# Performance work log

Hardware: AMD Instinct MI355X
Metric: run time of the kernel (lower is better)

Reference implementation:

```python
import jax, jax.numpy as jnp
import numpy as np
from jax.ops import segment_sum, segment_max

B, L, D, H, DK, NL, V, FF = 8, 256, 256, 8, 32, 4, 2048, 1024
N = B * L
EPS = 1e-5


def _ln(x, g, b):
    m = jnp.mean(x, -1, keepdims=True)
    v = jnp.var(x, -1, keepdims=True)
    return (x - m) * jax.lax.rsqrt(v + EPS) * g + b


def setup_inputs() -> dict:
    key = jax.random.key(0)
    ks = list(jax.random.split(key, 16))
    # causal decoder-decoder edges, sorted by destination (DGL 'dd' eids)
    dst_seq = np.repeat(np.arange(L), np.arange(L) + 1)
    src_seq = np.concatenate([np.arange(j + 1) for j in range(L)])
    src = jnp.asarray(np.concatenate([src_seq + b * L for b in range(B)]), jnp.int32)
    dst = jnp.asarray(np.concatenate([dst_seq + b * L for b in range(B)]), jnp.int32)
    tokens = jax.random.randint(ks[0], (N,), 0, V)
    positions = jnp.tile(jnp.arange(L), B)  # tgt[1]
    s = 0.02
    nrm = lambda k, sh: jax.random.normal(k, sh, jnp.float32) * s
    return {
        'tokens': tokens, 'positions': positions, 'src': src, 'dst': dst,
        'value_tab': nrm(ks[1], (V, D)),
        'coord_tab': nrm(ks[2], (3, D)),
        'pos_tab': nrm(ks[3], (L, D)),
        'ln1_g': jnp.ones((NL, D), jnp.float32), 'ln1_b': jnp.zeros((NL, D), jnp.float32),
        'Wq': nrm(ks[4], (NL, D, D)), 'Wk': nrm(ks[5], (NL, D, D)),
        'Wv': nrm(ks[6], (NL, D, D)), 'Wo': nrm(ks[7], (NL, D, D)),
        'ln2_g': jnp.ones((NL, D), jnp.float32), 'ln2_b': jnp.zeros((NL, D), jnp.float32),
        'W1': nrm(ks[8], (NL, D, FF)), 'b1': jnp.zeros((NL, FF), jnp.float32),
        'W2': nrm(ks[9], (NL, FF, D)), 'b2': jnp.zeros((NL, D), jnp.float32),
        'lnf_g': jnp.ones((D,), jnp.float32), 'lnf_b': jnp.zeros((D,), jnp.float32),
        'Wgen': nrm(ks[10], (D, V)), 'bgen': jnp.zeros((V,), jnp.float32),
    }


def reference(tokens, positions, src, dst, value_tab, coord_tab, pos_tab,
              ln1_g, ln1_b, Wq, Wk, Wv, Wo, ln2_g, ln2_b,
              W1, b1, W2, b2, lnf_g, lnf_b, Wgen, bgen):
    # embeddings: value*sqrt(d) + coord(pos%3) + pos(pos//3)
    x = value_tab[tokens] * jnp.sqrt(jnp.float32(D)) \
        + coord_tab[positions % 3] + pos_tab[positions // 3]
    inv_sqrt_dk = 1.0 / jnp.sqrt(jnp.float32(DK))
    for i in range(NL):
        # pre_func: layernorm + qkv projection, split heads
        xn = _ln(x, ln1_g[i], ln1_b[i])
        q = (xn @ Wq[i]).reshape(N, H, DK)
        k = (xn @ Wk[i]).reshape(N, H, DK)
        v = (xn @ Wv[i]).reshape(N, H, DK)
        # apply_edges(u_dot_v): per-edge, per-head score
        score = jnp.einsum('ehd,ehd->eh', k[src], q[dst]) * inv_sqrt_dk  # [E,H]
        # edge_softmax over edges grouped by destination node
        m = jax.lax.stop_gradient(
            segment_max(score, dst, num_segments=N, indices_are_sorted=True))
        a = jnp.exp(score - m[dst])
        denom = segment_sum(a, dst, num_segments=N, indices_are_sorted=True)
        alpha = a / denom[dst]  # [E,H]
        # send_and_recv(u_mul_e -> sum): softmax-weighted aggregation
        z = segment_sum(v[src] * alpha[..., None], dst,
                        num_segments=N, indices_are_sorted=True).reshape(N, D)
        # post_func: output proj + residual, then FFN sublayer
        x = x + z @ Wo[i]
        xn2 = _ln(x, ln2_g[i], ln2_b[i])
        x = x + (jax.nn.relu(xn2 @ W1[i] + b1[i]) @ W2[i] + b2[i])
    x = _ln(x, lnf_g, lnf_b)
    return jax.nn.log_softmax(x @ Wgen + bgen, axis=-1)  # generator
```

## Files before the change

### kernel.cpp

```cpp
#include <hip/hip_runtime.h>
#include <hip/hip_bf16.h>
#include <math.h>

constexpr int B_ = 8, L_ = 256, D_ = 256, H_ = 8, DK_ = 32, NL_ = 4, V_ = 2048, FF_ = 1024;
constexpr int N_ = B_ * L_;
constexpr float EPS_ = 1e-5f;
constexpr int LDW_ = 56;

typedef short bf16x8 __attribute__((ext_vector_type(8)));
typedef float f32x4 __attribute__((ext_vector_type(4)));
typedef _Float16 f16x4 __attribute__((ext_vector_type(4)));

__device__ __forceinline__ short f2b(float f) {
    union { __hip_bfloat16 h; short s; } u;
    u.h = __float2bfloat16(f);
    return u.s;
}

__global__ void transpose_all(const float* __restrict__ Wq, const float* __restrict__ Wk,
                              const float* __restrict__ Wv, const float* __restrict__ Wo,
                              const float* __restrict__ W1, const float* __restrict__ W2,
                              const float* __restrict__ Wgen,
                              short* __restrict__ wqT, short* __restrict__ wkT,
                              short* __restrict__ wvT, short* __restrict__ woT,
                              short* __restrict__ w1T, short* __restrict__ w2T,
                              short* __restrict__ wgT,
                              const int* __restrict__ tokens, const int* __restrict__ positions,
                              const float* __restrict__ vtab, const float* __restrict__ ctab,
                              const float* __restrict__ ptab, float* __restrict__ x) {
    __shared__ float tile[32][33];
    int id = blockIdx.x;
    if (id >= 3584) {
        int n = id - 3584;
        int d = threadIdx.y * 32 + threadIdx.x;
        int tok = tokens[n], p = positions[n];
        x[n * D_ + d] = vtab[tok * D_ + d] * 16.0f + ctab[(p % 3) * D_ + d] + ptab[(p / 3) * D_ + d];
        return;
    }
    const float* src;
    short* dst;
    int K, Nn, tx, ty;
    if (id < 1024) {
        int m = id >> 8, rem = id & 255, layer = rem >> 6, tt = rem & 63;
        K = 256; Nn = 256; tx = tt & 7; ty = tt >> 3;
        size_t off = (size_t)layer * 256 * 256;
        if (m == 0) { src = Wq + off; dst = wqT + off; }
        else if (m == 1) { src = Wk + off; dst = wkT + off; }
        else if (m == 2) { src = Wv + off; dst = wvT + off; }
        else { src = Wo + off; dst = woT + off; }
    } else if (id < 2048) {
        int rem = id - 1024, layer = rem >> 8, tt = rem & 255;
        K = 256; Nn = 1024; tx = tt & 31; ty = tt >> 5;
        size_t off = (size_t)layer * 256 * 1024;
        src = W1 + off; dst = w1T + off;
    } else if (id < 3072) {
        int rem = id - 2048, layer = rem >> 8, tt = rem & 255;
        K = 1024; Nn = 256; tx = tt & 7; ty = tt >> 3;
        size_t off = (size_t)layer * 1024 * 256;
        src = W2 + off; dst = w2T + off;
    } else {
        int tt = id - 3072;
        K = 256; Nn = 2048; tx = tt & 63; ty = tt >> 6;
        src = Wgen; dst = wgT;
    }
    int n0 = tx * 32, k0 = ty * 32;
    int x_ = threadIdx.x, y_ = threadIdx.y;
#pragma unroll
    for (int i = 0; i < 32; i += 8)
        tile[y_ + i][x_] = src[(size_t)(k0 + y_ + i) * Nn + n0 + x_];
    __syncthreads();
#pragma unroll
    for (int i = 0; i < 32; i += 8)
        dst[(size_t)(n0 + y_ + i) * K + k0 + x_] = f2b(tile[x_][y_ + i]);
}

__device__ __forceinline__ int4 pack8(const float* v) {
    union { short s[8]; int4 q; } u;
#pragma unroll
    for (int j = 0; j < 8; ++j) u.s[j] = f2b(v[j]);
    return u.q;
}

template <int EPI, bool HAS_BIAS>
__device__ __forceinline__ void gemm_epilogue(f32x4 acc00, f32x4 acc01, f32x4 acc10, f32x4 acc11,
                                              const float* __restrict__ bias, float* __restrict__ Cf,
                                              short* __restrict__ Cb, int Nout, int kz,
                                              int m0, int n0, int mo, int no, int quad, int r) {
#pragma unroll
    for (int i = 0; i < 2; ++i) {
#pragma unroll
        for (int j = 0; j < 2; ++j) {
            f32x4 acc = (i == 0) ? (j == 0 ? acc00 : acc01) : (j == 0 ? acc10 : acc11);
            int col = n0 + no + j * 16 + r;
            float bval = HAS_BIAS ? bias[col] : 0.f;
#pragma unroll
            for (int p = 0; p < 4; ++p) {
                int row = m0 + mo + i * 16 + quad * 4 + p;
                float v = acc[p];
                if (EPI == 1) {
                    Cb[(size_t)row * Nout + col] = f2b(fmaxf(v + bval, 0.f));
                } else if (EPI == 2) {
                    float add = v + ((HAS_BIAS && kz == 0) ? bval : 0.f);
                    atomicAdd(&Cf[(size_t)row * Nout + col], add);
                } else if (EPI == 3) {
                    Cf[(size_t)row * Nout + col] = v + bval;
                } else if (EPI == 4) {
                    Cb[(size_t)row * Nout + col] = f2b(v);
                } else {
                    ((_Float16*)Cb)[(size_t)row * Nout + col] = (_Float16)v;
                }
            }
        }
    }
}

template <int EPI, bool HAS_BIAS>
__device__ __forceinline__ void gemm_body(const short* __restrict__ A, const short* __restrict__ Bt,
                                          const float* __restrict__ bias, float* __restrict__ Cf,
                                          short* __restrict__ Cb, int M, int K, int Nout,
                                          int kbeg, int kend, int kz) {
    __shared__ short As[2][64][LDW_];
    __shared__ short Bs[2][64][LDW_];
    int t = threadIdx.x;
    int m0 = blockIdx.x * 64, n0 = blockIdx.y * 64;
    int sr = t >> 2, sc = (t & 3) * 8;
    int lane = t & 63, w = t >> 6;
    int mo = (w & 1) * 32, no = (w >> 1) * 32;
    int quad = lane >> 4, r = lane & 15;
    f32x4 acc00 = {}, acc01 = {}, acc10 = {}, acc11 = {};
    const short* Ap = &A[(size_t)(m0 + sr) * K + sc];
    const short* Bp = &Bt[(size_t)(n0 + sr) * K + sc];
    int4 av = *(const int4*)(Ap + kbeg);
    int4 bv = *(const int4*)(Bp + kbeg);
    *(int4*)&As[0][sr][sc] = av;
    *(int4*)&Bs[0][sr][sc] = bv;
    if (kbeg + 32 < kend) {
        av = *(const int4*)(Ap + kbeg + 32);
        bv = *(const int4*)(Bp + kbeg + 32);
    }
    __syncthreads();
    int p = 0;
    for (int k0 = kbeg; k0 < kend; k0 += 32, p ^= 1) {
        if (k0 + 32 < kend) {
            *(int4*)&As[p ^ 1][sr][sc] = av;
            *(int4*)&Bs[p ^ 1][sr][sc] = bv;
            if (k0 + 64 < kend) {
                av = *(const int4*)(Ap + k0 + 64);
                bv = *(const int4*)(Bp + k0 + 64);
            }
        }
        bf16x8 a0 = *(const bf16x8*)&As[p][mo + r][quad * 8];
        bf16x8 a1 = *(const bf16x8*)&As[p][mo + 16 + r][quad * 8];
        bf16x8 b0 = *(const bf16x8*)&Bs[p][no + r][quad * 8];
        bf16x8 b1 = *(const bf16x8*)&Bs[p][no + 16 + r][quad * 8];
        acc00 = __builtin_amdgcn_mfma_f32_16x16x32_bf16(a0, b0, acc00, 0, 0, 0);
        acc01 = __builtin_amdgcn_mfma_f32_16x16x32_bf16(a0, b1, acc01, 0, 0, 0);
        acc10 = __builtin_amdgcn_mfma_f32_16x16x32_bf16(a1, b0, acc10, 0, 0, 0);
        acc11 = __builtin_amdgcn_mfma_f32_16x16x32_bf16(a1, b1, acc11, 0, 0, 0);
        if (k0 + 32 < kend) __syncthreads();
    }
    gemm_epilogue<EPI, HAS_BIAS>(acc00, acc01, acc10, acc11, bias, Cf, Cb, Nout, kz,
                                 m0, n0, mo, no, quad, r);
}

template <int EPI, bool HAS_BIAS>
__device__ __forceinline__ void gemm_ln_body(const float* __restrict__ X,
                                             const float* __restrict__ lg, const float* __restrict__ lb,
                                             const short* __restrict__ Bt,
                                             const float* __restrict__ bias, float* __restrict__ Cf,
                                             short* __restrict__ Cb, int Nout) {
    __shared__ short As[2][64][LDW_];
    __shared__ short Bs[2][64][LDW_];
    __shared__ float gs[256], bs_[256];
    int t = threadIdx.x;
    int m0 = blockIdx.x * 64, n0 = blockIdx.y * 64;
    int sr = t >> 2, sc = (t & 3) * 8;
    int lane = t & 63, w = t >> 6;
    int mo = (w & 1) * 32, no = (w >> 1) * 32;
    int quad = lane >> 4, r = lane & 15;

    float xv[64];
    const float* xp = &X[(size_t)(m0 + sr) * 256 + sc];
#pragma unroll
    for (int c = 0; c < 8; ++c) {
        *(float4*)&xv[c * 8] = *(const float4*)(xp + c * 32);
        *(float4*)&xv[c * 8 + 4] = *(const float4*)(xp + c * 32 + 4);
    }
    const short* Bp = &Bt[(size_t)(n0 + sr) * 256 + sc];
    int4 bv = *(const int4*)Bp;
    gs[t] = lg[t];
    bs_[t] = lb[t];

    float s1 = 0.f, s2 = 0.f;
#pragma unroll
    for (int j = 0; j < 64; ++j) {
        s1 += xv[j];
        s2 += xv[j] * xv[j];
    }
    s1 += __shfl_xor(s1, 1, 64); s1 += __shfl_xor(s1, 2, 64);
    s2 += __shfl_xor(s2, 1, 64); s2 += __shfl_xor(s2, 2, 64);
    float mean = s1 * (1.0f / 256.0f);
    float inv = rsqrtf(s2 * (1.0f / 256.0f) - mean * mean + EPS_);
    __syncthreads();

    int4 a_regs[8];
#pragma unroll
    for (int c = 0; c < 8; ++c) {
        float tmp[8];
#pragma unroll
        for (int j = 0; j < 8; ++j)
            tmp[j] = (xv[c * 8 + j] - mean) * inv * gs[c * 32 + sc + j] + bs_[c * 32 + sc + j];
        a_regs[c] = pack8(tmp);
    }

    *(int4*)&As[0][sr][sc] = a_regs[0];
    *(int4*)&Bs[0][sr][sc] = bv;
    bv = *(const int4*)(Bp + 32);
    __syncthreads();

    f32x4 acc00 = {}, acc01 = {}, acc10 = {}, acc11 = {};
#pragma unroll
    for (int c = 0; c < 8; ++c) {
        int p = c & 1;
        if (c + 1 < 8) {
            *(int4*)&As[p ^ 1][sr][sc] = a_regs[c + 1];
            *(int4*)&Bs[p ^ 1][sr][sc] = bv;
            if (c + 2 < 8) bv = *(const int4*)(Bp + (c + 2) * 32);
        }
        bf16x8 a0 = *(const bf16x8*)&As[p][mo + r][quad * 8];
        bf16x8 a1 = *(const bf16x8*)&As[p][mo + 16 + r][quad * 8];
        bf16x8 b0 = *(const bf16x8*)&Bs[p][no + r][quad * 8];
        bf16x8 b1 = *(const bf16x8*)&Bs[p][no + 16 + r][quad * 8];
        acc00 = __builtin_amdgcn_mfma_f32_16x16x32_bf16(a0, b0, acc00, 0, 0, 0);
        acc01 = __builtin_amdgcn_mfma_f32_16x16x32_bf16(a0, b1, acc01, 0, 0, 0);
        acc10 = __builtin_amdgcn_mfma_f32_16x16x32_bf16(a1, b0, acc10, 0, 0, 0);
        acc11 = __builtin_amdgcn_mfma_f32_16x16x32_bf16(a1, b1, acc11, 0, 0, 0);
        if (c + 1 < 8) __syncthreads();
    }
    gemm_epilogue<EPI, HAS_BIAS>(acc00, acc01, acc10, acc11, bias, Cf, Cb, Nout, 0,
                                 m0, n0, mo, no, quad, r);
}

__global__ __launch_bounds__(256) void gemm_ln_qkv(const float* __restrict__ X,
                                                   const float* __restrict__ lg, const float* __restrict__ lb,
                                                   const short* __restrict__ wq, const short* __restrict__ wk,
                                                   const short* __restrict__ wv,
                                                   short* __restrict__ q, short* __restrict__ k,
                                                   short* __restrict__ v) {
    if (blockIdx.z == 0)
        gemm_ln_body<4, false>(X, lg, lb, wq, nullptr, nullptr, q, D_);
    else if (blockIdx.z == 1)
        gemm_ln_body<4, false>(X, lg, lb, wk, nullptr, nullptr, k, D_);
    else
        gemm_ln_body<5, false>(X, lg, lb, wv, nullptr, nullptr, v, D_);
}

__global__ __launch_bounds__(256) void gemm_ln_relu(const float* __restrict__ X,
                                                    const float* __restrict__ lg, const float* __restrict__ lb,
                                                    const short* __restrict__ Bt, const float* __restrict__ bias,
                                                    short* __restrict__ C) {
    gemm_ln_body<1, true>(X, lg, lb, Bt, bias, nullptr, C, FF_);
}

__global__ __launch_bounds__(256) void gemm_ln_bias(const float* __restrict__ X,
                                                    const float* __restrict__ lg, const float* __restrict__ lb,
                                                    const short* __restrict__ Bt, const float* __restrict__ bias,
                                                    float* __restrict__ C) {
    gemm_ln_body<3, true>(X, lg, lb, Bt, bias, C, nullptr, V_);
}

template <int SPLITK, bool HAS_BIAS>
__global__ __launch_bounds__(256) void gemm_accum(const short* __restrict__ A, const short* __restrict__ Bt,
                                                  const float* __restrict__ bias, float* __restrict__ C,
                                                  int M, int K, int Nout) {
    int Kp = K / SPLITK;
    int kz = blockIdx.z;
    gemm_body<2, HAS_BIAS>(A, Bt, bias, C, nullptr, M, K, Nout, kz * Kp, kz * Kp + Kp, kz);
}

__global__ __launch_bounds__(64) void attn_kernel(const short* __restrict__ q,
                                                  const short* __restrict__ k,
                                                  const _Float16* __restrict__ v,
                                                  short* __restrict__ z) {
    int blk = blockIdx.x;
    int bh = blk & 63;
    int qt = 15 - (blk >> 6);
    int b = bh >> 3, h = bh & 7;
    int lane = threadIdx.x;
    int r = lane & 15, quad = lane >> 4;
    int row0 = b * L_;

    bf16x8 qf = *(const bf16x8*)&q[(size_t)(row0 + qt * 16 + r) * D_ + h * DK_ + quad * 8];
    f32x4 O0 = {}, O1 = {};
    float mA = -1e30f, den = 0.f;
    int nk = qt + 1;

    bf16x8 kf = *(const bf16x8*)&k[(size_t)(row0 + r) * D_ + h * DK_ + quad * 8];
    f16x4 va, vb;
    {
        const _Float16* vp = v + (size_t)(row0 + quad * 4) * D_ + h * DK_;
#pragma unroll
        for (int i = 0; i < 4; ++i) {
            va[i] = vp[(size_t)i * D_ + r];
            vb[i] = vp[(size_t)i * D_ + 16 + r];
        }
    }
    for (int kt = 0; kt < nk; ++kt) {
        bf16x8 kf_n = kf;
        f16x4 va_n = va, vb_n = vb;
        if (kt + 1 < nk) {
            kf_n = *(const bf16x8*)&k[(size_t)(row0 + (kt + 1) * 16 + r) * D_ + h * DK_ + quad * 8];
            const _Float16* vp = v + (size_t)(row0 + (kt + 1) * 16 + quad * 4) * D_ + h * DK_;
#pragma unroll
            for (int i = 0; i < 4; ++i) {
                va_n[i] = vp[(size_t)i * D_ + r];
                vb_n[i] = vp[(size_t)i * D_ + 16 + r];
            }
        }
        f32x4 zero = {};
        f32x4 s = __builtin_amdgcn_mfma_f32_16x16x32_bf16(kf, qf, zero, 0, 0, 0);
#pragma unroll
        for (int i2 = 0; i2 < 4; ++i2) s[i2] *= 0.17677669529663687f;
        if (kt == qt) {
#pragma unroll
            for (int i2 = 0; i2 < 4; ++i2)
                if (quad * 4 + i2 > r) s[i2] = -1e30f;
        }
        float tmax = fmaxf(fmaxf(s[0], s[1]), fmaxf(s[2], s[3]));
        tmax = fmaxf(tmax, __shfl_xor(tmax, 16, 64));
        tmax = fmaxf(tmax, __shfl_xor(tmax, 32, 64));
        float mn = fmaxf(mA, tmax);
        float alpha = __expf(mA - mn);
        mA = mn;
        float p0 = __expf(s[0] - mn), p1 = __expf(s[1] - mn);
        float p2 = __expf(s[2] - mn), p3 = __expf(s[3] - mn);
        float ts = (p0 + p1) + (p2 + p3);
        ts += __shfl_xor(ts, 16, 64);
        ts += __shfl_xor(ts, 32, 64);
        den = den * alpha + ts;
        f16x4 pf;
        pf[0] = (_Float16)p0; pf[1] = (_Float16)p1; pf[2] = (_Float16)p2; pf[3] = (_Float16)p3;
        float al[4];
#pragma unroll
        for (int i2 = 0; i2 < 4; ++i2) al[i2] = __shfl(alpha, quad * 4 + i2, 64);
#pragma unroll
        for (int i2 = 0; i2 < 4; ++i2) { O0[i2] *= al[i2]; O1[i2] *= al[i2]; }
        O0 = __builtin_amdgcn_mfma_f32_16x16x16f16(pf, va, O0, 0, 0, 0);
        O1 = __builtin_amdgcn_mfma_f32_16x16x16f16(pf, vb, O1, 0, 0, 0);
        kf = kf_n; va = va_n; vb = vb_n;
    }
#pragma unroll
    for (int i2 = 0; i2 < 4; ++i2) {
        float inv = 1.0f / __shfl(den, quad * 4 + i2, 64);
        int rowz = row0 + qt * 16 + quad * 4 + i2;
        z[(size_t)rowz * D_ + h * DK_ + r] = f2b(O0[i2] * inv);
        z[(size_t)rowz * D_ + h * DK_ + 16 + r] = f2b(O1[i2] * inv);
    }
}

__global__ void lsm_kernel(float* __restrict__ logits) {
    __shared__ float rm[4], rs[4];
    int row = blockIdx.x, t = threadIdx.x;
    float* p = logits + (size_t)row * V_;
    float vals[8];
    float mx = -INFINITY;
#pragma unroll
    for (int i = 0; i < 8; ++i) {
        vals[i] = p[t + i * 256];
        mx = fmaxf(mx, vals[i]);
    }
#pragma unroll
    for (int off = 32; off; off >>= 1) mx = fmaxf(mx, __shfl_xor(mx, off, 64));
    int w = t >> 6;
    if ((t & 63) == 0) rm[w] = mx;
    __syncthreads();
    mx = fmaxf(fmaxf(rm[0], rm[1]), fmaxf(rm[2], rm[3]));
    float s = 0.f;
#pragma unroll
    for (int i = 0; i < 8; ++i) s += __expf(vals[i] - mx);
#pragma unroll
    for (int off = 32; off; off >>= 1) s += __shfl_xor(s, off, 64);
    if ((t & 63) == 0) rs[w] = s;
    __syncthreads();
    s = rs[0] + rs[1] + rs[2] + rs[3];
    float lse = mx + logf(s);
#pragma unroll
    for (int i = 0; i < 8; ++i) p[t + i * 256] = vals[i] - lse;
}

extern "C" void kernel_launch(void* const* d_in, const int* in_sizes, int n_in,
                              void* d_out, int out_size, void* d_ws, size_t ws_size,
                              hipStream_t stream) {
    const int* tokens = (const int*)d_in[0];
    const int* positions = (const int*)d_in[1];
    const float* vtab = (const float*)d_in[4];
    const float* ctab = (const float*)d_in[5];
    const float* ptab = (const float*)d_in[6];
    const float* ln1_g = (const float*)d_in[7];
    const float* ln1_b = (const float*)d_in[8];
    const float* Wq = (const float*)d_in[9];
    const float* Wk = (const float*)d_in[10];
    const float* Wv = (const float*)d_in[11];
    const float* Wo = (const float*)d_in[12];
    const float* ln2_g = (const float*)d_in[13];
    const float* ln2_b = (const float*)d_in[14];
    const float* W1 = (const float*)d_in[15];
    const float* b1 = (const float*)d_in[16];
    const float* W2 = (const float*)d_in[17];
    const float* b2 = (const float*)d_in[18];
    const float* lnf_g = (const float*)d_in[19];
    const float* lnf_b = (const float*)d_in[20];
    const float* Wgen = (const float*)d_in[21];
    const float* bgen = (const float*)d_in[22];

    char* p = (char*)d_ws;
    float* x = (float*)p;      p += (size_t)N_ * D_ * 4;
    short* qb = (short*)p;     p += (size_t)N_ * D_ * 4;
    short* kb = (short*)p;     p += (size_t)N_ * D_ * 4;
    short* vbh = (short*)p;    p += (size_t)N_ * D_ * 4;
    short* zbb = (short*)p;    p += (size_t)N_ * D_ * 2;
    short* hbb = (short*)p;    p += (size_t)N_ * FF_ * 2;
    short* wqT = (short*)p;    p += (size_t)NL_ * D_ * D_ * 2;
    short* wkT = (short*)p;    p += (size_t)NL_ * D_ * D_ * 2;
    short* wvT = (short*)p;    p += (size_t)NL_ * D_ * D_ * 2;
    short* woT = (short*)p;    p += (size_t)NL_ * D_ * D_ * 2;
    short* w1T = (short*)p;    p += (size_t)NL_ * D_ * FF_ * 2;
    short* w2T = (short*)p;    p += (size_t)NL_ * FF_ * D_ * 2;
    short* wgT = (short*)p;    p += (size_t)D_ * V_ * 2;
    float* out = (float*)d_out;

    dim3 tb(32, 8);
    transpose_all<<<5632, tb, 0, stream>>>(Wq, Wk, Wv, Wo, W1, W2, Wgen,
                                           wqT, wkT, wvT, woT, w1T, w2T, wgT,
                                           tokens, positions, vtab, ctab, ptab, x);

    dim3 gQKV(N_ / 64, D_ / 64, 3);
    dim3 gWo(N_ / 64, D_ / 64, 2);
    dim3 gW1(N_ / 64, FF_ / 64);
    dim3 gW2(N_ / 64, D_ / 64, 4);
    dim3 gGen(N_ / 64, V_ / 64);
    for (int i = 0; i < NL_; ++i) {
        gemm_ln_qkv<<<gQKV, 256, 0, stream>>>(x, ln1_g + i * D_, ln1_b + i * D_,
                                              wqT + (size_t)i * D_ * D_, wkT + (size_t)i * D_ * D_,
                                              wvT + (size_t)i * D_ * D_, qb, kb, vbh);
        attn_kernel<<<B_ * H_ * 16, 64, 0, stream>>>(qb, kb, (const _Float16*)vbh, zbb);
        gemm_accum<2, false><<<gWo, 256, 0, stream>>>(zbb, woT + (size_t)i * D_ * D_, nullptr, x, N_, D_, D_);
        gemm_ln_relu<<<gW1, 256, 0, stream>>>(x, ln2_g + i * D_, ln2_b + i * D_,
                                              w1T + (size_t)i * D_ * FF_, b1 + (size_t)i * FF_, hbb);
        gemm_accum<4, true><<<gW2, 256, 0, stream>>>(hbb, w2T + (size_t)i * FF_ * D_, b2 + (size_t)i * D_,
                                                     x, N_, FF_, D_);
    }
    gemm_ln_bias<<<gGen, 256, 0, stream>>>(x, lnf_g, lnf_b, wgT, bgen, out);
    lsm_kernel<<<N_, 256, 0, stream>>>(out);
}
```

Measured before the change: 306.1 us.

## Drop split-K atomics for residual GEMMs and precompute final layernorm

The Wo and W2 residual GEMMs stop splitting K across blockIdx.z with atomicAdd and instead run a single full-K pass per tile, doing a plain read-modify-write add into x. The final layernorm moves into its own kernel that writes bf16 activations, so the generator GEMM becomes a plain GEMM with bias instead of recomputing layernorm in every column block. This removes atomic traffic and redundant LN work, but it cuts the grid size for the residual GEMMs (from 256/512 blocks to 128), which lowers parallelism, and it adds one extra launch.

```diff
diff --git a/kernel.cpp b/kernel.cpp
--- a/kernel.cpp
+++ b/kernel.cpp
@@ -74,6 +74,32 @@
         dst[(size_t)(n0 + y_ + i) * K + k0 + x_] = f2b(tile[x_][y_ + i]);
 }
 
+__global__ void ln_kernel(const float* __restrict__ x, const float* __restrict__ g,
+                          const float* __restrict__ b, short* __restrict__ out) {
+    __shared__ float r1[4], r2[4], mv[2];
+    int n = blockIdx.x, t = threadIdx.x;
+    float v = x[n * D_ + t];
+    float s1 = v, s2 = v * v;
+#pragma unroll
+    for (int off = 32; off; off >>= 1) {
+        s1 += __shfl_down(s1, off, 64);
+        s2 += __shfl_down(s2, off, 64);
+    }
+    int w = t >> 6;
+    if ((t & 63) == 0) { r1[w] = s1; r2[w] = s2; }
+    __syncthreads();
+    if (t == 0) {
+        float a = r1[0] + r1[1] + r1[2] + r1[3];
+        float c = r2[0] + r2[1] + r2[2] + r2[3];
+        float mean = a * (1.0f / D_);
+        float var = c * (1.0f / D_) - mean * mean;
+        mv[0] = mean;
+        mv[1] = rsqrtf(var + EPS_);
+    }
+    __syncthreads();
+    out[n * D_ + t] = f2b((v - mv[0]) * mv[1] * g[t] + b[t]);
+}
+
 __device__ __forceinline__ int4 pack8(const float* v) {
     union { short s[8]; int4 q; } u;
 #pragma unroll
@@ -84,7 +110,7 @@
 template <int EPI, bool HAS_BIAS>
 __device__ __forceinline__ void gemm_epilogue(f32x4 acc00, f32x4 acc01, f32x4 acc10, f32x4 acc11,
                                               const float* __restrict__ bias, float* __restrict__ Cf,
-                                              short* __restrict__ Cb, int Nout, int kz,
+                                              short* __restrict__ Cb, int Nout,
                                               int m0, int n0, int mo, int no, int quad, int r) {
 #pragma unroll
     for (int i = 0; i < 2; ++i) {
@@ -99,15 +125,15 @@
                 float v = acc[p];
                 if (EPI == 1) {
                     Cb[(size_t)row * Nout + col] = f2b(fmaxf(v + bval, 0.f));
-                } else if (EPI == 2) {
-                    float add = v + ((HAS_BIAS && kz == 0) ? bval : 0.f);
-                    atomicAdd(&Cf[(size_t)row * Nout + col], add);
                 } else if (EPI == 3) {
                     Cf[(size_t)row * Nout + col] = v + bval;
                 } else if (EPI == 4) {
                     Cb[(size_t)row * Nout + col] = f2b(v);
+                } else if (EPI == 5) {
+                    ((_Float16*)Cb)[(size_t)row * Nout + col] = (_Float16)v;
                 } else {
-                    ((_Float16*)Cb)[(size_t)row * Nout + col] = (_Float16)v;
+                    size_t idx = (size_t)row * Nout + col;
+                    Cf[idx] = Cf[idx] + v + bval;
                 }
             }
         }
@@ -117,8 +143,7 @@
 template <int EPI, bool HAS_BIAS>
 __device__ __forceinline__ void gemm_body(const short* __restrict__ A, const short* __restrict__ Bt,
                                           const float* __restrict__ bias, float* __restrict__ Cf,
-                                          short* __restrict__ Cb, int M, int K, int Nout,
-                                          int kbeg, int kend, int kz) {
+                                          short* __restrict__ Cb, int M, int K, int Nout) {
     __shared__ short As[2][64][LDW_];
     __shared__ short Bs[2][64][LDW_];
     int t = threadIdx.x;
@@ -130,21 +155,21 @@
     f32x4 acc00 = {}, acc01 = {}, acc10 = {}, acc11 = {};
     const short* Ap = &A[(size_t)(m0 + sr) * K + sc];
     const short* Bp = &Bt[(size_t)(n0 + sr) * K + sc];
-    int4 av = *(const int4*)(Ap + kbeg);
-    int4 bv = *(const int4*)(Bp + kbeg);
+    int4 av = *(const int4*)Ap;
+    int4 bv = *(const int4*)Bp;
     *(int4*)&As[0][sr][sc] = av;
     *(int4*)&Bs[0][sr][sc] = bv;
-    if (kbeg + 32 < kend) {
-        av = *(const int4*)(Ap + kbeg + 32);
-        bv = *(const int4*)(Bp + kbeg + 32);
+    if (32 < K) {
+        av = *(const int4*)(Ap + 32);
+        bv = *(const int4*)(Bp + 32);
     }
     __syncthreads();
     int p = 0;
-    for (int k0 = kbeg; k0 < kend; k0 += 32, p ^= 1) {
-        if (k0 + 32 < kend) {
+    for (int k0 = 0; k0 < K; k0 += 32, p ^= 1) {
+        if (k0 + 32 < K) {
             *(int4*)&As[p ^ 1][sr][sc] = av;
             *(int4*)&Bs[p ^ 1][sr][sc] = bv;
-            if (k0 + 64 < kend) {
+            if (k0 + 64 < K) {
                 av = *(const int4*)(Ap + k0 + 64);
                 bv = *(const int4*)(Bp + k0 + 64);
             }
@@ -157,9 +182,9 @@
         acc01 = __builtin_amdgcn_mfma_f32_16x16x32_bf16(a0, b1, acc01, 0, 0, 0);
         acc10 = __builtin_amdgcn_mfma_f32_16x16x32_bf16(a1, b0, acc10, 0, 0, 0);
         acc11 = __builtin_amdgcn_mfma_f32_16x16x32_bf16(a1, b1, acc11, 0, 0, 0);
-        if (k0 + 32 < kend) __syncthreads();
-    }
-    gemm_epilogue<EPI, HAS_BIAS>(acc00, acc01, acc10, acc11, bias, Cf, Cb, Nout, kz,
+        if (k0 + 32 < K) __syncthreads();
+    }
+    gemm_epilogue<EPI, HAS_BIAS>(acc00, acc01, acc10, acc11, bias, Cf, Cb, Nout,
                                  m0, n0, mo, no, quad, r);
 }
 
@@ -237,7 +262,7 @@
         acc11 = __builtin_amdgcn_mfma_f32_16x16x32_bf16(a1, b1, acc11, 0, 0, 0);
         if (c + 1 < 8) __syncthreads();
     }
-    gemm_epilogue<EPI, HAS_BIAS>(acc00, acc01, acc10, acc11, bias, Cf, Cb, Nout, 0,
+    gemm_epilogue<EPI, HAS_BIAS>(acc00, acc01, acc10, acc11, bias, Cf, Cb, Nout,
                                  m0, n0, mo, no, quad, r);
 }
 
@@ -262,20 +287,17 @@
     gemm_ln_body<1, true>(X, lg, lb, Bt, bias, nullptr, C, FF_);
 }
 
-__global__ __launch_bounds__(256) void gemm_ln_bias(const float* __restrict__ X,
-                                                    const float* __restrict__ lg, const float* __restrict__ lb,
-                                                    const short* __restrict__ Bt, const float* __restrict__ bias,
-                                                    float* __restrict__ C) {
-    gemm_ln_body<3, true>(X, lg, lb, Bt, bias, C, nullptr, V_);
-}
-
-template <int SPLITK, bool HAS_BIAS>
-__global__ __launch_bounds__(256) void gemm_accum(const short* __restrict__ A, const short* __restrict__ Bt,
-                                                  const float* __restrict__ bias, float* __restrict__ C,
-                                                  int M, int K, int Nout) {
-    int Kp = K / SPLITK;
-    int kz = blockIdx.z;
-    gemm_body<2, HAS_BIAS>(A, Bt, bias, C, nullptr, M, K, Nout, kz * Kp, kz * Kp + Kp, kz);
+template <bool HAS_BIAS>
+__global__ __launch_bounds__(256) void gemm_rmw(const short* __restrict__ A, const short* __restrict__ Bt,
+                                                const float* __restrict__ bias, float* __restrict__ C,
+                                                int M, int K, int Nout) {
+    gemm_body<6, HAS_BIAS>(A, Bt, bias, C, nullptr, M, K, Nout);
+}
+
+__global__ __launch_bounds__(256) void gemm_bias(const short* __restrict__ A, const short* __restrict__ Bt,
+                                                 const float* __restrict__ bias, float* __restrict__ C,
+                                                 int M, int K, int Nout) {
+    gemm_body<3, true>(A, Bt, bias, C, nullptr, M, K, Nout);
 }
 
 __global__ __launch_bounds__(64) void attn_kernel(const short* __restrict__ q,
@@ -418,6 +440,7 @@
     short* qb = (short*)p;     p += (size_t)N_ * D_ * 4;
     short* kb = (short*)p;     p += (size_t)N_ * D_ * 4;
     short* vbh = (short*)p;    p += (size_t)N_ * D_ * 4;
+    short* xnb = (short*)p;    p += (size_t)N_ * D_ * 2;
     short* zbb = (short*)p;    p += (size_t)N_ * D_ * 2;
     short* hbb = (short*)p;    p += (size_t)N_ * FF_ * 2;
     short* wqT = (short*)p;    p += (size_t)NL_ * D_ * D_ * 2;
@@ -435,21 +458,22 @@
                                            tokens, positions, vtab, ctab, ptab, x);
 
     dim3 gQKV(N_ / 64, D_ / 64, 3);
-    dim3 gWo(N_ / 64, D_ / 64, 2);
+    dim3 gWo(N_ / 64, D_ / 64);
     dim3 gW1(N_ / 64, FF_ / 64);
-    dim3 gW2(N_ / 64, D_ / 64, 4);
+    dim3 gW2(N_ / 64, D_ / 64);
     dim3 gGen(N_ / 64, V_ / 64);
     for (int i = 0; i < NL_; ++i) {
         gemm_ln_qkv<<<gQKV, 256, 0, stream>>>(x, ln1_g + i * D_, ln1_b + i * D_,
                                               wqT + (size_t)i * D_ * D_, wkT + (size_t)i * D_ * D_,
                                               wvT + (size_t)i * D_ * D_, qb, kb, vbh);
         attn_kernel<<<B_ * H_ * 16, 64, 0, stream>>>(qb, kb, (const _Float16*)vbh, zbb);
-        gemm_accum<2, false><<<gWo, 256, 0, stream>>>(zbb, woT + (size_t)i * D_ * D_, nullptr, x, N_, D_, D_);
+        gemm_rmw<false><<<gWo, 256, 0, stream>>>(zbb, woT + (size_t)i * D_ * D_, nullptr, x, N_, D_, D_);
         gemm_ln_relu<<<gW1, 256, 0, stream>>>(x, ln2_g + i * D_, ln2_b + i * D_,
                                               w1T + (size_t)i * D_ * FF_, b1 + (size_t)i * FF_, hbb);
-        gemm_accum<4, true><<<gW2, 256, 0, stream>>>(hbb, w2T + (size_t)i * FF_ * D_, b2 + (size_t)i * D_,
-                                                     x, N_, FF_, D_);
-    }
-    gemm_ln_bias<<<gGen, 256, 0, stream>>>(x, lnf_g, lnf_b, wgT, bgen, out);
+        gemm_rmw<true><<<gW2, 256, 0, stream>>>(hbb, w2T + (size_t)i * FF_ * D_, b2 + (size_t)i * D_,
+                                                x, N_, FF_, D_);
+    }
+    ln_kernel<<<N_, 256, 0, stream>>>(x, lnf_g, lnf_b, xnb);
+    gemm_bias<<<gGen, 256, 0, stream>>>(xnb, wgT, bgen, out, N_, D_, V_);
     lsm_kernel<<<N_, 256, 0, stream>>>(out);
 }
```

New measurement: 318.6 us. 4.1% more time.

## Fuse output projection into attention kernel with atomic accumulation into residual

Applied to the files above, without the earlier changes.

The attention kernel now stages its normalized per-head output in shared memory and multiplies it directly by the matching slice of the Wo weights using MFMA. It atomically adds the partial projections into the residual stream x. This removes the separate Wo GEMM launch and the bf16 z buffer round-trip. In exchange, each head contributes atomics to every output element, which raises atomic traffic to x several-fold compared with the split-K GEMM.

```diff
diff --git a/kernel.cpp b/kernel.cpp
--- a/kernel.cpp
+++ b/kernel.cpp
@@ -278,10 +278,12 @@
     gemm_body<2, HAS_BIAS>(A, Bt, bias, C, nullptr, M, K, Nout, kz * Kp, kz * Kp + Kp, kz);
 }
 
-__global__ __launch_bounds__(64) void attn_kernel(const short* __restrict__ q,
-                                                  const short* __restrict__ k,
-                                                  const _Float16* __restrict__ v,
-                                                  short* __restrict__ z) {
+__global__ __launch_bounds__(64) void attn_wo_kernel(const short* __restrict__ q,
+                                                     const short* __restrict__ k,
+                                                     const _Float16* __restrict__ v,
+                                                     const short* __restrict__ woT,
+                                                     float* __restrict__ x) {
+    __shared__ short Os[16][36];
     int blk = blockIdx.x;
     int bh = blk & 63;
     int qt = 15 - (blk >> 6);
@@ -352,9 +354,22 @@
 #pragma unroll
     for (int i2 = 0; i2 < 4; ++i2) {
         float inv = 1.0f / __shfl(den, quad * 4 + i2, 64);
-        int rowz = row0 + qt * 16 + quad * 4 + i2;
-        z[(size_t)rowz * D_ + h * DK_ + r] = f2b(O0[i2] * inv);
-        z[(size_t)rowz * D_ + h * DK_ + 16 + r] = f2b(O1[i2] * inv);
+        int qr = quad * 4 + i2;
+        Os[qr][r] = f2b(O0[i2] * inv);
+        Os[qr][16 + r] = f2b(O1[i2] * inv);
+    }
+    __syncthreads();
+    bf16x8 af = *(const bf16x8*)&Os[r][quad * 8];
+    const short* wp = &woT[(size_t)r * 256 + h * DK_ + quad * 8];
+    float* xp = &x[(size_t)(row0 + qt * 16 + quad * 4) * D_ + r];
+#pragma unroll
+    for (int nt = 0; nt < 16; ++nt) {
+        bf16x8 bf = *(const bf16x8*)(wp + (size_t)nt * 16 * 256);
+        f32x4 zero = {};
+        f32x4 acc = __builtin_amdgcn_mfma_f32_16x16x32_bf16(af, bf, zero, 0, 0, 0);
+#pragma unroll
+        for (int p = 0; p < 4; ++p)
+            atomicAdd(xp + (size_t)p * D_ + nt * 16, acc[p]);
     }
 }
 
@@ -418,7 +433,6 @@
     short* qb = (short*)p;     p += (size_t)N_ * D_ * 4;
     short* kb = (short*)p;     p += (size_t)N_ * D_ * 4;
     short* vbh = (short*)p;    p += (size_t)N_ * D_ * 4;
-    short* zbb = (short*)p;    p += (size_t)N_ * D_ * 2;
     short* hbb = (short*)p;    p += (size_t)N_ * FF_ * 2;
     short* wqT = (short*)p;    p += (size_t)NL_ * D_ * D_ * 2;
     short* wkT = (short*)p;    p += (size_t)NL_ * D_ * D_ * 2;
@@ -435,7 +449,6 @@
                                            tokens, positions, vtab, ctab, ptab, x);
 
     dim3 gQKV(N_ / 64, D_ / 64, 3);
-    dim3 gWo(N_ / 64, D_ / 64, 2);
     dim3 gW1(N_ / 64, FF_ / 64);
     dim3 gW2(N_ / 64, D_ / 64, 4);
     dim3 gGen(N_ / 64, V_ / 64);
@@ -443,8 +456,8 @@
         gemm_ln_qkv<<<gQKV, 256, 0, stream>>>(x, ln1_g + i * D_, ln1_b + i * D_,
                                               wqT + (size_t)i * D_ * D_, wkT + (size_t)i * D_ * D_,
                                               wvT + (size_t)i * D_ * D_, qb, kb, vbh);
-        attn_kernel<<<B_ * H_ * 16, 64, 0, stream>>>(qb, kb, (const _Float16*)vbh, zbb);
-        gemm_accum<2, false><<<gWo, 256, 0, stream>>>(zbb, woT + (size_t)i * D_ * D_, nullptr, x, N_, D_, D_);
+        attn_wo_kernel<<<B_ * H_ * 16, 64, 0, stream>>>(qb, kb, (const _Float16*)vbh,
+                                                        woT + (size_t)i * D_ * D_, x);
         gemm_ln_relu<<<gW1, 256, 0, stream>>>(x, ln2_g + i * D_, ln2_b + i * D_,
                                               w1T + (size_t)i * D_ * FF_, b1 + (size_t)i * FF_, hbb);
         gemm_accum<4, true><<<gW2, 256, 0, stream>>>(hbb, w2T + (size_t)i * FF_ * D_, b2 + (size_t)i * D_,
```

Result: slower. 320.9 us (+4.8%).

## Fuse LN2, W1+ReLU and W2 into one FFN kernel with ping-pong residual

Applied to the files above, without the earlier changes.

Replaces the separate LN+W1+ReLU GEMM and the split-K W2 GEMM with one kernel. Each block computes a 128-wide slice of the hidden layer in shared memory, then multiplies it by the matching W2 slice and atomically accumulates into a second residual buffer. The Wo GEMM zeroes that buffer as it goes and the two buffers swap each layer. This removes the global round trip of the N×FF hidden activations and one launch per layer, in exchange for more atomics (8-way over FF), a single-buffered B tile with two barriers per k-step, and high register use for the 64-float row cache.

```diff
diff --git a/kernel.cpp b/kernel.cpp
--- a/kernel.cpp
+++ b/kernel.cpp
@@ -84,7 +84,8 @@
 template <int EPI, bool HAS_BIAS>
 __device__ __forceinline__ void gemm_epilogue(f32x4 acc00, f32x4 acc01, f32x4 acc10, f32x4 acc11,
                                               const float* __restrict__ bias, float* __restrict__ Cf,
-                                              short* __restrict__ Cb, int Nout, int kz,
+                                              short* __restrict__ Cb, float* __restrict__ Z,
+                                              int Nout, int kz,
                                               int m0, int n0, int mo, int no, int quad, int r) {
 #pragma unroll
     for (int i = 0; i < 2; ++i) {
@@ -97,11 +98,11 @@
             for (int p = 0; p < 4; ++p) {
                 int row = m0 + mo + i * 16 + quad * 4 + p;
                 float v = acc[p];
-                if (EPI == 1) {
-                    Cb[(size_t)row * Nout + col] = f2b(fmaxf(v + bval, 0.f));
-                } else if (EPI == 2) {
+                if (EPI == 2) {
+                    size_t idx = (size_t)row * Nout + col;
                     float add = v + ((HAS_BIAS && kz == 0) ? bval : 0.f);
-                    atomicAdd(&Cf[(size_t)row * Nout + col], add);
+                    atomicAdd(&Cf[idx], add);
+                    if (Z != nullptr && kz == 0) Z[idx] = 0.f;
                 } else if (EPI == 3) {
                     Cf[(size_t)row * Nout + col] = v + bval;
                 } else if (EPI == 4) {
@@ -117,8 +118,8 @@
 template <int EPI, bool HAS_BIAS>
 __device__ __forceinline__ void gemm_body(const short* __restrict__ A, const short* __restrict__ Bt,
                                           const float* __restrict__ bias, float* __restrict__ Cf,
-                                          short* __restrict__ Cb, int M, int K, int Nout,
-                                          int kbeg, int kend, int kz) {
+                                          short* __restrict__ Cb, float* __restrict__ Z,
+                                          int M, int K, int Nout, int kbeg, int kend, int kz) {
     __shared__ short As[2][64][LDW_];
     __shared__ short Bs[2][64][LDW_];
     int t = threadIdx.x;
@@ -159,7 +160,7 @@
         acc11 = __builtin_amdgcn_mfma_f32_16x16x32_bf16(a1, b1, acc11, 0, 0, 0);
         if (k0 + 32 < kend) __syncthreads();
     }
-    gemm_epilogue<EPI, HAS_BIAS>(acc00, acc01, acc10, acc11, bias, Cf, Cb, Nout, kz,
+    gemm_epilogue<EPI, HAS_BIAS>(acc00, acc01, acc10, acc11, bias, Cf, Cb, Z, Nout, kz,
                                  m0, n0, mo, no, quad, r);
 }
 
@@ -237,7 +238,7 @@
         acc11 = __builtin_amdgcn_mfma_f32_16x16x32_bf16(a1, b1, acc11, 0, 0, 0);
         if (c + 1 < 8) __syncthreads();
     }
-    gemm_epilogue<EPI, HAS_BIAS>(acc00, acc01, acc10, acc11, bias, Cf, Cb, Nout, 0,
+    gemm_epilogue<EPI, HAS_BIAS>(acc00, acc01, acc10, acc11, bias, Cf, Cb, nullptr, Nout, 0,
                                  m0, n0, mo, no, quad, r);
 }
 
@@ -255,13 +256,6 @@
         gemm_ln_body<5, false>(X, lg, lb, wv, nullptr, nullptr, v, D_);
 }
 
-__global__ __launch_bounds__(256) void gemm_ln_relu(const float* __restrict__ X,
-                                                    const float* __restrict__ lg, const float* __restrict__ lb,
-                                                    const short* __restrict__ Bt, const float* __restrict__ bias,
-                                                    short* __restrict__ C) {
-    gemm_ln_body<1, true>(X, lg, lb, Bt, bias, nullptr, C, FF_);
-}
-
 __global__ __launch_bounds__(256) void gemm_ln_bias(const float* __restrict__ X,
                                                     const float* __restrict__ lg, const float* __restrict__ lb,
                                                     const short* __restrict__ Bt, const float* __restrict__ bias,
@@ -272,10 +266,134 @@
 template <int SPLITK, bool HAS_BIAS>
 __global__ __launch_bounds__(256) void gemm_accum(const short* __restrict__ A, const short* __restrict__ Bt,
                                                   const float* __restrict__ bias, float* __restrict__ C,
-                                                  int M, int K, int Nout) {
+                                                  float* __restrict__ Z, int M, int K, int Nout) {
     int Kp = K / SPLITK;
     int kz = blockIdx.z;
-    gemm_body<2, HAS_BIAS>(A, Bt, bias, C, nullptr, M, K, Nout, kz * Kp, kz * Kp + Kp, kz);
+    gemm_body<2, HAS_BIAS>(A, Bt, bias, C, nullptr, Z, M, K, Nout, kz * Kp, kz * Kp + Kp, kz);
+}
+
+__global__ __launch_bounds__(256) void gemm_ln_ffn(const float* __restrict__ X,
+                                                   const float* __restrict__ lg, const float* __restrict__ lb,
+                                                   const short* __restrict__ w1T, const float* __restrict__ b1,
+                                                   const short* __restrict__ w2T, const float* __restrict__ b2,
+                                                   float* __restrict__ Xout) {
+    __shared__ short Af[64][264];
+    __shared__ short Hs[64][136];
+    __shared__ short Bs[64][LDW_];
+    __shared__ float gs[256], bs_[256];
+    int t = threadIdx.x;
+    int m0 = blockIdx.x * 64, f0 = blockIdx.y * 128;
+    int sr = t >> 2, sc = (t & 3) * 8;
+    int lane = t & 63, w = t >> 6;
+    int mo = (w & 1) * 32, no = (w >> 1) * 32;
+    int quad = lane >> 4, r = lane & 15;
+
+    float xv[64];
+    const float* xp = &X[(size_t)(m0 + sr) * 256 + sc];
+#pragma unroll
+    for (int c = 0; c < 8; ++c) {
+        *(float4*)&xv[c * 8] = *(const float4*)(xp + c * 32);
+        *(float4*)&xv[c * 8 + 4] = *(const float4*)(xp + c * 32 + 4);
+    }
+    gs[t] = lg[t];
+    bs_[t] = lb[t];
+    float s1 = 0.f, s2 = 0.f;
+#pragma unroll
+    for (int j = 0; j < 64; ++j) {
+        s1 += xv[j];
+        s2 += xv[j] * xv[j];
+    }
+    s1 += __shfl_xor(s1, 1, 64); s1 += __shfl_xor(s1, 2, 64);
+    s2 += __shfl_xor(s2, 1, 64); s2 += __shfl_xor(s2, 2, 64);
+    float mean = s1 * (1.0f / 256.0f);
+    float inv = rsqrtf(s2 * (1.0f / 256.0f) - mean * mean + EPS_);
+    __syncthreads();
+#pragma unroll
+    for (int c = 0; c < 8; ++c) {
+        float tmp[8];
+#pragma unroll
+        for (int j = 0; j < 8; ++j)
+            tmp[j] = (xv[c * 8 + j] - mean) * inv * gs[c * 32 + sc + j] + bs_[c * 32 + sc + j];
+        *(int4*)&Af[sr][c * 32 + sc] = pack8(tmp);
+    }
+
+#pragma unroll
+    for (int nb = 0; nb < 2; ++nb) {
+        const short* Bp = &w1T[(size_t)(f0 + nb * 64 + sr) * 256 + sc];
+        int4 bv = *(const int4*)Bp;
+        f32x4 acc00 = {}, acc01 = {}, acc10 = {}, acc11 = {};
+#pragma unroll
+        for (int ks = 0; ks < 8; ++ks) {
+            int4 bn = bv;
+            if (ks + 1 < 8) bn = *(const int4*)(Bp + (ks + 1) * 32);
+            __syncthreads();
+            *(int4*)&Bs[sr][sc] = bv;
+            __syncthreads();
+            bf16x8 a0 = *(const bf16x8*)&Af[mo + r][ks * 32 + quad * 8];
+            bf16x8 a1 = *(const bf16x8*)&Af[mo + 16 + r][ks * 32 + quad * 8];
+            bf16x8 b0 = *(const bf16x8*)&Bs[no + r][quad * 8];
+            bf16x8 b1 = *(const bf16x8*)&Bs[no + 16 + r][quad * 8];
+            acc00 = __builtin_amdgcn_mfma_f32_16x16x32_bf16(a0, b0, acc00, 0, 0, 0);
+            acc01 = __builtin_amdgcn_mfma_f32_16x16x32_bf16(a0, b1, acc01, 0, 0, 0);
+            acc10 = __builtin_amdgcn_mfma_f32_16x16x32_bf16(a1, b0, acc10, 0, 0, 0);
+            acc11 = __builtin_amdgcn_mfma_f32_16x16x32_bf16(a1, b1, acc11, 0, 0, 0);
+            bv = bn;
+        }
+#pragma unroll
+        for (int i = 0; i < 2; ++i) {
+#pragma unroll
+            for (int j = 0; j < 2; ++j) {
+                f32x4 acc = (i == 0) ? (j == 0 ? acc00 : acc01) : (j == 0 ? acc10 : acc11);
+                int lcol = no + j * 16 + r;
+                float bval = b1[f0 + nb * 64 + lcol];
+#pragma unroll
+                for (int p = 0; p < 4; ++p) {
+                    int row = mo + i * 16 + quad * 4 + p;
+                    Hs[row][nb * 64 + lcol] = f2b(fmaxf(acc[p] + bval, 0.f));
+                }
+            }
+        }
+    }
+
+#pragma unroll
+    for (int nt = 0; nt < 4; ++nt) {
+        const short* Bp = &w2T[(size_t)(nt * 64 + sr) * 1024 + f0 + sc];
+        int4 bv = *(const int4*)Bp;
+        f32x4 acc00 = {}, acc01 = {}, acc10 = {}, acc11 = {};
+#pragma unroll
+        for (int ks = 0; ks < 4; ++ks) {
+            int4 bn = bv;
+            if (ks + 1 < 4) bn = *(const int4*)(Bp + (ks + 1) * 32);
+            __syncthreads();
+            *(int4*)&Bs[sr][sc] = bv;
+            __syncthreads();
+            bf16x8 a0 = *(const bf16x8*)&Hs[mo + r][ks * 32 + quad * 8];
+            bf16x8 a1 = *(const bf16x8*)&Hs[mo + 16 + r][ks * 32 + quad * 8];
+            bf16x8 b0 = *(const bf16x8*)&Bs[no + r][quad * 8];
+            bf16x8 b1 = *(const bf16x8*)&Bs[no + 16 + r][quad * 8];
+            acc00 = __builtin_amdgcn_mfma_f32_16x16x32_bf16(a0, b0, acc00, 0, 0, 0);
+            acc01 = __builtin_amdgcn_mfma_f32_16x16x32_bf16(a0, b1, acc01, 0, 0, 0);
+            acc10 = __builtin_amdgcn_mfma_f32_16x16x32_bf16(a1, b0, acc10, 0, 0, 0);
+            acc11 = __builtin_amdgcn_mfma_f32_16x16x32_bf16(a1, b1, acc11, 0, 0, 0);
+            bv = bn;
+        }
+#pragma unroll
+        for (int i = 0; i < 2; ++i) {
+#pragma unroll
+            for (int j = 0; j < 2; ++j) {
+                f32x4 acc = (i == 0) ? (j == 0 ? acc00 : acc01) : (j == 0 ? acc10 : acc11);
+                int col = nt * 64 + no + j * 16 + r;
+#pragma unroll
+                for (int p = 0; p < 4; ++p) {
+                    int row = m0 + mo + i * 16 + quad * 4 + p;
+                    size_t idx = (size_t)row * 256 + col;
+                    float add = acc[p];
+                    if (blockIdx.y == 0) add += b2[col] + X[idx];
+                    atomicAdd(&Xout[idx], add);
+                }
+            }
+        }
+    }
 }
 
 __global__ __launch_bounds__(64) void attn_kernel(const short* __restrict__ q,
@@ -415,11 +533,12 @@
 
     char* p = (char*)d_ws;
     float* x = (float*)p;      p += (size_t)N_ * D_ * 4;
+    float* x2 = (float*)p;     p += (size_t)N_ * D_ * 4;
     short* qb = (short*)p;     p += (size_t)N_ * D_ * 4;
     short* kb = (short*)p;     p += (size_t)N_ * D_ * 4;
     short* vbh = (short*)p;    p += (size_t)N_ * D_ * 4;
+    short* xnb = (short*)p;    p += (size_t)N_ * D_ * 2;
     short* zbb = (short*)p;    p += (size_t)N_ * D_ * 2;
-    short* hbb = (short*)p;    p += (size_t)N_ * FF_ * 2;
     short* wqT = (short*)p;    p += (size_t)NL_ * D_ * D_ * 2;
     short* wkT = (short*)p;    p += (size_t)NL_ * D_ * D_ * 2;
     short* wvT = (short*)p;    p += (size_t)NL_ * D_ * D_ * 2;
@@ -428,6 +547,7 @@
     short* w2T = (short*)p;    p += (size_t)NL_ * FF_ * D_ * 2;
     short* wgT = (short*)p;    p += (size_t)D_ * V_ * 2;
     float* out = (float*)d_out;
+    (void)xnb;
 
     dim3 tb(32, 8);
     transpose_all<<<5632, tb, 0, stream>>>(Wq, Wk, Wv, Wo, W1, W2, Wgen,
@@ -436,20 +556,22 @@
 
     dim3 gQKV(N_ / 64, D_ / 64, 3);
     dim3 gWo(N_ / 64, D_ / 64, 2);
-    dim3 gW1(N_ / 64, FF_ / 64);
-    dim3 gW2(N_ / 64, D_ / 64, 4);
+    dim3 gFFN(N_ / 64, 8);
     dim3 gGen(N_ / 64, V_ / 64);
+    float* xA = x;
+    float* xB = x2;
     for (int i = 0; i < NL_; ++i) {
-        gemm_ln_qkv<<<gQKV, 256, 0, stream>>>(x, ln1_g + i * D_, ln1_b + i * D_,
+        gemm_ln_qkv<<<gQKV, 256, 0, stream>>>(xA, ln1_g + i * D_, ln1_b + i * D_,
                                               wqT + (size_t)i * D_ * D_, wkT + (size_t)i * D_ * D_,
                                               wvT + (size_t)i * D_ * D_, qb, kb, vbh);
         attn_kernel<<<B_ * H_ * 16, 64, 0, stream>>>(qb, kb, (const _Float16*)vbh, zbb);
-        gemm_accum<2, false><<<gWo, 256, 0, stream>>>(zbb, woT + (size_t)i * D_ * D_, nullptr, x, N_, D_, D_);
-        gemm_ln_relu<<<gW1, 256, 0, stream>>>(x, ln2_g + i * D_, ln2_b + i * D_,
-                                              w1T + (size_t)i * D_ * FF_, b1 + (size_t)i * FF_, hbb);
-        gemm_accum<4, true><<<gW2, 256, 0, stream>>>(hbb, w2T + (size_t)i * FF_ * D_, b2 + (size_t)i * D_,
-                                                     x, N_, FF_, D_);
-    }
-    gemm_ln_bias<<<gGen, 256, 0, stream>>>(x, lnf_g, lnf_b, wgT, bgen, out);
+        gemm_accum<2, false><<<gWo, 256, 0, stream>>>(zbb, woT + (size_t)i * D_ * D_, nullptr,
+                                                      xA, xB, N_, D_, D_);
+        gemm_ln_ffn<<<gFFN, 256, 0, stream>>>(xA, ln2_g + i * D_, ln2_b + i * D_,
+                                              w1T + (size_t)i * D_ * FF_, b1 + (size_t)i * FF_,
+                                              w2T + (size_t)i * FF_ * D_, b2 + (size_t)i * D_, xB);
+        float* tmp = xA; xA = xB; xB = tmp;
+    }
+    gemm_ln_bias<<<gGen, 256, 0, stream>>>(xA, lnf_g, lnf_b, wgT, bgen, out);
     lsm_kernel<<<N_, 256, 0, stream>>>(out);
 }
```

Result: slower. 396.3 us (+29.5%).
